# Kernel optimization log

Hardware: AMD Instinct MI355X
Metric: run time of the kernel (lower is better)

Reference implementation:

```python
import jax, jax.numpy as jnp
import numpy as np

ALPHA = 0.1
BETA = float(np.log(0.5 / 4 + 1.0))  # theta=0.5, layer=4


def setup_inputs() -> dict:
    key = jax.random.key(0)
    k = jax.random.split(key, 6)
    B, C, N, K = 1, 128, 40000, 16
    x = jax.random.normal(k[0], (B, C, N, 1), dtype=jnp.float32)
    x_0 = jax.random.normal(k[1], (B, N, C), dtype=jnp.float32)
    edge_index = jax.random.randint(k[2], (2, B, N, K), 0, N)
    W1 = jax.random.normal(k[3], (C, C), dtype=jnp.float32) * 0.05
    W2 = jax.random.normal(k[4], (C, C), dtype=jnp.float32) * 0.05
    bias = jax.random.uniform(k[5], (1, 1, C), dtype=jnp.float32)
    return {"x": x, "x_0": x_0, "edge_index": edge_index, "W1": W1, "W2": W2, "bias": bias}


def reference(x, x_0, edge_index, W1, W2, bias):
    # x: [B, C, N, 1]; x_0: [B, N, C]; edge_index: [2, B, N, K]
    B, C, N, _ = x.shape
    idx = edge_index[0]  # neighbor indices [B, N, K]
    self_idx = jnp.broadcast_to(jnp.arange(N, dtype=idx.dtype)[None, :, None], (B, N, 1))
    idx = jnp.concatenate([idx, self_idx], axis=-1)  # add self loops -> [B, N, K+1]
    deg = idx.shape[-1]  # constant degree K+1
    x2 = x[..., 0]  # [B, C, N]
    # irregular gather of neighbor features: [B, C, N, K+1]
    x_j = jax.vmap(lambda xb, ib: xb[:, ib])(x2, idx)
    aggr = x_j.sum(axis=-1) * (1.0 / deg)  # [B, C, N]
    aggr = jnp.swapaxes(aggr, 1, 2)  # [B, N, C]
    out = (aggr * ((1.0 - ALPHA) * (1.0 - BETA))
           + jnp.einsum('bnc,oc->bno', aggr, W1) * BETA
           + x_0 * (ALPHA * (1.0 - BETA))
           + jnp.einsum('bnc,oc->bno', x_0, W2) * BETA
           + bias)
    out = jax.nn.relu(out)
    return jnp.swapaxes(out, 1, 2)[..., None]  # [B, C, N, 1]
```

## Files before the change

kernel.cpp:

```cpp
#include <hip/hip_runtime.h>

#define N_NODES 40000
#define C_DIM   128
#define K_NBR   16

static constexpr float BETA_F  = 0.11778303565638346f;
static constexpr float C1_F    = 0.7939952679092549f;
static constexpr float C2_F    = 0.08822169643436166f;
static constexpr float INV_DEG = 1.0f / 17.0f;

typedef __attribute__((ext_vector_type(8))) short bf16x8;
typedef __attribute__((ext_vector_type(4))) float f32x4;

__device__ __forceinline__ unsigned pack_bf16x2(float a, float b) {
    unsigned ua = __float_as_uint(a), ub = __float_as_uint(b);
    ua += 0x7fffu + ((ua >> 16) & 1u);
    ub += 0x7fffu + ((ub >> 16) & 1u);
    return (ua >> 16) | (ub & 0xffff0000u);
}
__device__ __forceinline__ float bflo(unsigned u) { return __uint_as_float(u << 16); }
__device__ __forceinline__ float bfhi(unsigned u) { return __uint_as_float(u & 0xffff0000u); }

__global__ __launch_bounds__(256) void prep_kernel(
        const float* __restrict__ x,
        const float* __restrict__ W1,
        const float* __restrict__ W2,
        unsigned* __restrict__ xTb,
        unsigned short* __restrict__ WB) {
    __shared__ unsigned lds[32 * 65];

    const int b = blockIdx.x;
    const int tid = threadIdx.x;

    if (b < 128) {
        const int i = b * 256 + tid;
        const int frag = i >> 9, within = i & 511;
        const int lane = within >> 3, j = within & 7;
        const int otile = frag >> 3, kblk = frag & 7;
        const int o = otile * 16 + (lane & 15);
        const int c = kblk * 32 + ((lane >> 4) << 3) + j;
        float v;
        if (c < 128) {
            v = (BETA_F * W1[o * 128 + c] + (c == o ? C1_F : 0.0f)) * INV_DEG;
        } else {
            const int c2 = c - 128;
            v = BETA_F * W2[o * 128 + c2] + (c2 == o ? C2_F : 0.0f);
        }
        unsigned u = __float_as_uint(v);
        u += 0x7fffu + ((u >> 16) & 1u);
        WB[i] = (unsigned short)(u >> 16);
        return;
    }

    const int nb = (b - 128) * 32;

    const int c2 = tid >> 2;
    const int h  = tid & 3;
    const float* r0 = &x[(size_t)(2 * c2)     * N_NODES + nb + h * 8];
    const float* r1 = &x[(size_t)(2 * c2 + 1) * N_NODES + nb + h * 8];
    const float4 a0 = *(const float4*)(r0);
    const float4 a1 = *(const float4*)(r0 + 4);
    const float4 b0 = *(const float4*)(r1);
    const float4 b1 = *(const float4*)(r1 + 4);

    unsigned* lrow = &lds[h * 8 * 65 + c2];
    lrow[0 * 65] = pack_bf16x2(a0.x, b0.x);
    lrow[1 * 65] = pack_bf16x2(a0.y, b0.y);
    lrow[2 * 65] = pack_bf16x2(a0.z, b0.z);
    lrow[3 * 65] = pack_bf16x2(a0.w, b0.w);
    lrow[4 * 65] = pack_bf16x2(a1.x, b1.x);
    lrow[5 * 65] = pack_bf16x2(a1.y, b1.y);
    lrow[6 * 65] = pack_bf16x2(a1.z, b1.z);
    lrow[7 * 65] = pack_bf16x2(a1.w, b1.w);
    __syncthreads();

    const int n = tid >> 3, q = tid & 7;
    const unsigned* src = &lds[n * 65 + q * 8];
    unsigned* dst = &xTb[(size_t)(nb + n) * 64 + q * 8];
    *(uint4*)&dst[0] = make_uint4(src[0], src[1], src[2], src[3]);
    *(uint4*)&dst[4] = make_uint4(src[4], src[5], src[6], src[7]);
}

__global__ __launch_bounds__(256) void fused3_kernel(
        const unsigned* __restrict__ xTb,
        const float*    __restrict__ x0,
        const int*      __restrict__ e0,
        const bf16x8*   __restrict__ WB,
        const float*    __restrict__ bias,
        float*          __restrict__ out) {
    __shared__ unsigned y[32][132];
    __shared__ int eis[512];

    const int nb   = blockIdx.x * 32;
    const int tid  = threadIdx.x;
    const int lane = tid & 63;
    const int wid  = tid >> 6;

    eis[tid]       = e0[(size_t)nb * K_NBR + tid];
    eis[256 + tid] = e0[(size_t)nb * K_NBR + 256 + tid];
    __syncthreads();

    const int h  = lane >> 5;
    const int l5 = lane & 31;
#pragma unroll 2
    for (int p4 = 0; p4 < 4; ++p4) {
        const int local = wid * 8 + p4 * 2 + h;
        const int n = nb + local;
        const uint2 sv = *(const uint2*)&xTb[(size_t)n * 64 + 2 * l5];
        float a0 = bflo(sv.x), a1 = bfhi(sv.x);
        float a2 = bflo(sv.y), a3 = bfhi(sv.y);
        const int* ep = &eis[local * K_NBR];
#pragma unroll
        for (int k = 0; k < K_NBR; ++k) {
            const int j = ep[k];
            const uint2 v = *(const uint2*)&xTb[(size_t)j * 64 + 2 * l5];
            a0 += bflo(v.x); a1 += bfhi(v.x);
            a2 += bflo(v.y); a3 += bfhi(v.y);
        }
        *(uint2*)&y[local][2 * l5] =
            make_uint2(pack_bf16x2(a0, a1), pack_bf16x2(a2, a3));
        const float4 xv = *(const float4*)&x0[(size_t)n * C_DIM + 4 * l5];
        *(uint2*)&y[local][64 + 2 * l5] =
            make_uint2(pack_bf16x2(xv.x, xv.y), pack_bf16x2(xv.z, xv.w));
    }
    __syncthreads();

    const int nh = wid & 1;
    const int oh = wid >> 1;
    const int arow = nh * 16 + (lane & 15);
    const int acol = (lane >> 4) * 4;

    bf16x8 afrag[8];
#pragma unroll
    for (int kb = 0; kb < 8; ++kb)
        afrag[kb] = *(const bf16x8*)&y[arow][kb * 16 + acol];

    f32x4 acc[4];
#pragma unroll
    for (int t = 0; t < 4; ++t) {
        f32x4 a = {0.f, 0.f, 0.f, 0.f};
#pragma unroll
        for (int kb = 0; kb < 8; ++kb) {
            bf16x8 bv = WB[((oh * 4 + t) * 8 + kb) * 64 + lane];
            a = __builtin_amdgcn_mfma_f32_16x16x32_bf16(afrag[kb], bv, a, 0, 0, 0);
        }
        acc[t] = a;
    }

    const int rbase = nh * 16 + (lane >> 4) * 4;
#pragma unroll
    for (int t = 0; t < 4; ++t) {
        const int o = oh * 64 + t * 16 + (lane & 15);
        const float bo = bias[o];
        float4 res;
        res.x = fmaxf(acc[t][0] + bo, 0.0f);
        res.y = fmaxf(acc[t][1] + bo, 0.0f);
        res.z = fmaxf(acc[t][2] + bo, 0.0f);
        res.w = fmaxf(acc[t][3] + bo, 0.0f);
        *(float4*)&out[(size_t)o * N_NODES + nb + rbase] = res;
    }
}

extern "C" void kernel_launch(void* const* d_in, const int* in_sizes, int n_in,
                              void* d_out, int out_size, void* d_ws, size_t ws_size,
                              hipStream_t stream) {
    const float* x    = (const float*)d_in[0];
    const float* x0   = (const float*)d_in[1];
    const int*   ei   = (const int*)  d_in[2];
    const float* W1   = (const float*)d_in[3];
    const float* W2   = (const float*)d_in[4];
    const float* bias = (const float*)d_in[5];
    float* out = (float*)d_out;

    unsigned short* WB  = (unsigned short*)d_ws;
    unsigned*       xTb = (unsigned*)((char*)d_ws + 65536);

    hipLaunchKernelGGL(prep_kernel, dim3(1378), dim3(256), 0, stream,
                       x, W1, W2, xTb, WB);
    hipLaunchKernelGGL(fused3_kernel, dim3(1250), dim3(256), 0, stream,
                       xTb, x0, ei, (const bf16x8*)WB, bias, out);
}
```

Baseline: 40.86 us.

## Apply W1 before the gather so aggregation sums transformed features

Uses linearity to compute z1 = x·(βW1ᵀ/17 + c·I) per node first in the prep kernel, then gathers and sums z1 over neighbours. The second kernel only does the x0·W2 GEMM, with K halved, then adds the gathered sum. Weights are now converted to bf16 on the fly from fp32 in each block instead of in a separate prep pass, and the output is staged in LDS for coalesced transposed stores. This trades a larger first kernel, with an MFMA and per-block weight loads, for dropping the separate weight-packing step and halving the second GEMM. It also adds an extra LDS round trip and rounds the transformed features to bf16 before aggregation.

```diff
diff --git a/kernel.cpp b/kernel.cpp
--- a/kernel.cpp
+++ b/kernel.cpp
@@ -7,7 +7,10 @@
 static constexpr float BETA_F  = 0.11778303565638346f;
 static constexpr float C1_F    = 0.7939952679092549f;
 static constexpr float C2_F    = 0.08822169643436166f;
-static constexpr float INV_DEG = 1.0f / 17.0f;
+static constexpr float SCALE_X  = BETA_F / 17.0f;
+static constexpr float SCALE_X0 = BETA_F;
+static constexpr float CD1_F = C1_F / BETA_F;
+static constexpr float CD2_F = C2_F / BETA_F;
 
 typedef __attribute__((ext_vector_type(8))) short bf16x8;
 typedef __attribute__((ext_vector_type(4))) float f32x4;
@@ -21,143 +24,197 @@
 __device__ __forceinline__ float bflo(unsigned u) { return __uint_as_float(u << 16); }
 __device__ __forceinline__ float bfhi(unsigned u) { return __uint_as_float(u & 0xffff0000u); }
 
-__global__ __launch_bounds__(256) void prep_kernel(
+__device__ __forceinline__ bf16x8 pack_w8(const float* wp) {
+    const float4 wa = *(const float4*)wp;
+    const float4 wb = *(const float4*)(wp + 4);
+    unsigned u[4];
+    u[0] = pack_bf16x2(wa.x, wa.y);
+    u[1] = pack_bf16x2(wa.z, wa.w);
+    u[2] = pack_bf16x2(wb.x, wb.y);
+    u[3] = pack_bf16x2(wb.z, wb.w);
+    uint4 uu = make_uint4(u[0], u[1], u[2], u[3]);
+    return *(bf16x8*)&uu;
+}
+
+__global__ __launch_bounds__(256) void z1_kernel(
         const float* __restrict__ x,
         const float* __restrict__ W1,
-        const float* __restrict__ W2,
-        unsigned* __restrict__ xTb,
-        unsigned short* __restrict__ WB) {
-    __shared__ unsigned lds[32 * 65];
-
-    const int b = blockIdx.x;
+        unsigned* __restrict__ z1T) {
+    __shared__ unsigned xs[32 * 68];
+
+    const int nb  = blockIdx.x * 32;
     const int tid = threadIdx.x;
 
-    if (b < 128) {
-        const int i = b * 256 + tid;
-        const int frag = i >> 9, within = i & 511;
-        const int lane = within >> 3, j = within & 7;
-        const int otile = frag >> 3, kblk = frag & 7;
-        const int o = otile * 16 + (lane & 15);
-        const int c = kblk * 32 + ((lane >> 4) << 3) + j;
-        float v;
-        if (c < 128) {
-            v = (BETA_F * W1[o * 128 + c] + (c == o ? C1_F : 0.0f)) * INV_DEG;
-        } else {
-            const int c2 = c - 128;
-            v = BETA_F * W2[o * 128 + c2] + (c2 == o ? C2_F : 0.0f);
-        }
-        unsigned u = __float_as_uint(v);
-        u += 0x7fffu + ((u >> 16) & 1u);
-        WB[i] = (unsigned short)(u >> 16);
-        return;
-    }
-
-    const int nb = (b - 128) * 32;
-
-    const int c2 = tid >> 2;
-    const int h  = tid & 3;
-    const float* r0 = &x[(size_t)(2 * c2)     * N_NODES + nb + h * 8];
-    const float* r1 = &x[(size_t)(2 * c2 + 1) * N_NODES + nb + h * 8];
-    const float4 a0 = *(const float4*)(r0);
-    const float4 a1 = *(const float4*)(r0 + 4);
-    const float4 b0 = *(const float4*)(r1);
-    const float4 b1 = *(const float4*)(r1 + 4);
-
-    unsigned* lrow = &lds[h * 8 * 65 + c2];
-    lrow[0 * 65] = pack_bf16x2(a0.x, b0.x);
-    lrow[1 * 65] = pack_bf16x2(a0.y, b0.y);
-    lrow[2 * 65] = pack_bf16x2(a0.z, b0.z);
-    lrow[3 * 65] = pack_bf16x2(a0.w, b0.w);
-    lrow[4 * 65] = pack_bf16x2(a1.x, b1.x);
-    lrow[5 * 65] = pack_bf16x2(a1.y, b1.y);
-    lrow[6 * 65] = pack_bf16x2(a1.z, b1.z);
-    lrow[7 * 65] = pack_bf16x2(a1.w, b1.w);
-    __syncthreads();
-
-    const int n = tid >> 3, q = tid & 7;
-    const unsigned* src = &lds[n * 65 + q * 8];
-    unsigned* dst = &xTb[(size_t)(nb + n) * 64 + q * 8];
-    *(uint4*)&dst[0] = make_uint4(src[0], src[1], src[2], src[3]);
-    *(uint4*)&dst[4] = make_uint4(src[4], src[5], src[6], src[7]);
-}
-
-__global__ __launch_bounds__(256) void fused3_kernel(
-        const unsigned* __restrict__ xTb,
-        const float*    __restrict__ x0,
-        const int*      __restrict__ e0,
-        const bf16x8*   __restrict__ WB,
-        const float*    __restrict__ bias,
-        float*          __restrict__ out) {
-    __shared__ unsigned y[32][132];
-    __shared__ int eis[512];
-
-    const int nb   = blockIdx.x * 32;
-    const int tid  = threadIdx.x;
+    {
+        const int c2 = tid >> 2;
+        const int h  = tid & 3;
+        const float* r0 = &x[(size_t)(2 * c2)     * N_NODES + nb + h * 8];
+        const float* r1 = &x[(size_t)(2 * c2 + 1) * N_NODES + nb + h * 8];
+        const float4 a0 = *(const float4*)(r0);
+        const float4 a1 = *(const float4*)(r0 + 4);
+        const float4 b0 = *(const float4*)(r1);
+        const float4 b1 = *(const float4*)(r1 + 4);
+        unsigned* lr = &xs[(h * 8) * 68 + c2];
+        lr[0 * 68] = pack_bf16x2(a0.x * SCALE_X, b0.x * SCALE_X);
+        lr[1 * 68] = pack_bf16x2(a0.y * SCALE_X, b0.y * SCALE_X);
+        lr[2 * 68] = pack_bf16x2(a0.z * SCALE_X, b0.z * SCALE_X);
+        lr[3 * 68] = pack_bf16x2(a0.w * SCALE_X, b0.w * SCALE_X);
+        lr[4 * 68] = pack_bf16x2(a1.x * SCALE_X, b1.x * SCALE_X);
+        lr[5 * 68] = pack_bf16x2(a1.y * SCALE_X, b1.y * SCALE_X);
+        lr[6 * 68] = pack_bf16x2(a1.z * SCALE_X, b1.z * SCALE_X);
+        lr[7 * 68] = pack_bf16x2(a1.w * SCALE_X, b1.w * SCALE_X);
+    }
+    __syncthreads();
+
     const int lane = tid & 63;
     const int wid  = tid >> 6;
+    const int nh = wid & 1, oh = wid >> 1;
+    const int arow = nh * 16 + (lane & 15);
+    const int acol = (lane >> 4) * 4;
+
+    bf16x8 af[4];
+#pragma unroll
+    for (int kb = 0; kb < 4; ++kb)
+        af[kb] = *(const bf16x8*)&xs[arow * 68 + kb * 16 + acol];
+
+    const int ob = oh * 64 + (lane & 15);
+    const int cb = (lane >> 4) * 8;
+    const int rbase = nh * 16 + (lane >> 4) * 4;
+    const bool hi = (lane & 1) != 0;
+
+#pragma unroll
+    for (int t = 0; t < 4; ++t) {
+        const int o = ob + t * 16;
+        f32x4 a = {0.f, 0.f, 0.f, 0.f};
+#pragma unroll
+        for (int kb = 0; kb < 4; ++kb) {
+            const bf16x8 bw = pack_w8(&W1[(size_t)o * C_DIM + kb * 32 + cb]);
+            a = __builtin_amdgcn_mfma_f32_16x16x32_bf16(af[kb], bw, a, 0, 0, 0);
+        }
+#pragma unroll
+        for (int r = 0; r < 4; ++r) {
+            const int row = rbase + r;
+            const unsigned ux = xs[row * 68 + (o >> 1)];
+            float v = a[r] + CD1_F * (hi ? bfhi(ux) : bflo(ux));
+            const float vp = __shfl_xor(v, 1);
+            if (!hi) {
+                z1T[(size_t)(nb + row) * 64 + (o >> 1)] = pack_bf16x2(v, vp);
+            }
+        }
+    }
+}
+
+__global__ __launch_bounds__(256) void gather_kernel(
+        const unsigned* __restrict__ z1T,
+        const float*    __restrict__ x0,
+        const float*    __restrict__ W2,
+        const float*    __restrict__ bias,
+        const int*      __restrict__ e0,
+        float*          __restrict__ out) {
+    __shared__ int      eis[512];
+    __shared__ unsigned x0s[32 * 68];
+    __shared__ float    zbuf[32 * 132];
+
+    const int nb  = blockIdx.x * 32;
+    const int tid = threadIdx.x;
+    const int lane = tid & 63;
+    const int wid  = tid >> 6;
 
     eis[tid]       = e0[(size_t)nb * K_NBR + tid];
     eis[256 + tid] = e0[(size_t)nb * K_NBR + 256 + tid];
-    __syncthreads();
-
-    const int h  = lane >> 5;
-    const int l5 = lane & 31;
-#pragma unroll 2
-    for (int p4 = 0; p4 < 4; ++p4) {
-        const int local = wid * 8 + p4 * 2 + h;
+
+    {
+        const int n = tid >> 3, g = tid & 7;
+        const float* r = &x0[(size_t)(nb + n) * C_DIM + g * 16];
+        const float4 v0 = *(const float4*)(r);
+        const float4 v1 = *(const float4*)(r + 4);
+        const float4 v2 = *(const float4*)(r + 8);
+        const float4 v3 = *(const float4*)(r + 12);
+        uint4 ua, ub;
+        ua.x = pack_bf16x2(v0.x * SCALE_X0, v0.y * SCALE_X0);
+        ua.y = pack_bf16x2(v0.z * SCALE_X0, v0.w * SCALE_X0);
+        ua.z = pack_bf16x2(v1.x * SCALE_X0, v1.y * SCALE_X0);
+        ua.w = pack_bf16x2(v1.z * SCALE_X0, v1.w * SCALE_X0);
+        ub.x = pack_bf16x2(v2.x * SCALE_X0, v2.y * SCALE_X0);
+        ub.y = pack_bf16x2(v2.z * SCALE_X0, v2.w * SCALE_X0);
+        ub.z = pack_bf16x2(v3.x * SCALE_X0, v3.y * SCALE_X0);
+        ub.w = pack_bf16x2(v3.z * SCALE_X0, v3.w * SCALE_X0);
+        *(uint4*)&x0s[n * 68 + g * 8]     = ua;
+        *(uint4*)&x0s[n * 68 + g * 8 + 4] = ub;
+    }
+    __syncthreads();
+
+    const int nh = wid & 1, oh = wid >> 1;
+    const int arow = nh * 16 + (lane & 15);
+    const int acol = (lane >> 4) * 4;
+    bf16x8 af[4];
+#pragma unroll
+    for (int kb = 0; kb < 4; ++kb)
+        af[kb] = *(const bf16x8*)&x0s[arow * 68 + kb * 16 + acol];
+
+    const int ob = oh * 64 + (lane & 15);
+    const int cb = (lane >> 4) * 8;
+    f32x4 acc[4];
+#pragma unroll
+    for (int t = 0; t < 4; ++t) {
+        f32x4 a = {0.f, 0.f, 0.f, 0.f};
+#pragma unroll
+        for (int kb = 0; kb < 4; ++kb) {
+            const bf16x8 bw = pack_w8(&W2[(size_t)(ob + t * 16) * C_DIM + kb * 32 + cb]);
+            a = __builtin_amdgcn_mfma_f32_16x16x32_bf16(af[kb], bw, a, 0, 0, 0);
+        }
+        acc[t] = a;
+    }
+
+    const int hw = tid >> 5, l5 = tid & 31;
+#pragma unroll 1
+    for (int p = 0; p < 4; ++p) {
+        const int local = hw * 4 + p;
         const int n = nb + local;
-        const uint2 sv = *(const uint2*)&xTb[(size_t)n * 64 + 2 * l5];
-        float a0 = bflo(sv.x), a1 = bfhi(sv.x);
-        float a2 = bflo(sv.y), a3 = bfhi(sv.y);
+        const uint2 sv = *(const uint2*)&z1T[(size_t)n * 64 + 2 * l5];
+        float s0 = bflo(sv.x), s1 = bfhi(sv.x);
+        float s2 = bflo(sv.y), s3 = bfhi(sv.y);
         const int* ep = &eis[local * K_NBR];
 #pragma unroll
         for (int k = 0; k < K_NBR; ++k) {
             const int j = ep[k];
-            const uint2 v = *(const uint2*)&xTb[(size_t)j * 64 + 2 * l5];
-            a0 += bflo(v.x); a1 += bfhi(v.x);
-            a2 += bflo(v.y); a3 += bfhi(v.y);
-        }
-        *(uint2*)&y[local][2 * l5] =
-            make_uint2(pack_bf16x2(a0, a1), pack_bf16x2(a2, a3));
-        const float4 xv = *(const float4*)&x0[(size_t)n * C_DIM + 4 * l5];
-        *(uint2*)&y[local][64 + 2 * l5] =
-            make_uint2(pack_bf16x2(xv.x, xv.y), pack_bf16x2(xv.z, xv.w));
-    }
-    __syncthreads();
-
-    const int nh = wid & 1;
-    const int oh = wid >> 1;
-    const int arow = nh * 16 + (lane & 15);
-    const int acol = (lane >> 4) * 4;
-
-    bf16x8 afrag[8];
-#pragma unroll
-    for (int kb = 0; kb < 8; ++kb)
-        afrag[kb] = *(const bf16x8*)&y[arow][kb * 16 + acol];
-
-    f32x4 acc[4];
+            const uint2 v = *(const uint2*)&z1T[(size_t)j * 64 + 2 * l5];
+            s0 += bflo(v.x); s1 += bfhi(v.x);
+            s2 += bflo(v.y); s3 += bfhi(v.y);
+        }
+        *(f32x4*)&zbuf[local * 132 + 4 * l5] = (f32x4){s0, s1, s2, s3};
+    }
+    __syncthreads();
+
+    const int rbase = nh * 16 + (lane >> 4) * 4;
+    const bool hi = (lane & 1) != 0;
 #pragma unroll
     for (int t = 0; t < 4; ++t) {
-        f32x4 a = {0.f, 0.f, 0.f, 0.f};
-#pragma unroll
-        for (int kb = 0; kb < 8; ++kb) {
-            bf16x8 bv = WB[((oh * 4 + t) * 8 + kb) * 64 + lane];
-            a = __builtin_amdgcn_mfma_f32_16x16x32_bf16(afrag[kb], bv, a, 0, 0, 0);
-        }
-        acc[t] = a;
-    }
-
-    const int rbase = nh * 16 + (lane >> 4) * 4;
-#pragma unroll
-    for (int t = 0; t < 4; ++t) {
-        const int o = oh * 64 + t * 16 + (lane & 15);
+        const int o = ob + t * 16;
         const float bo = bias[o];
-        float4 res;
-        res.x = fmaxf(acc[t][0] + bo, 0.0f);
-        res.y = fmaxf(acc[t][1] + bo, 0.0f);
-        res.z = fmaxf(acc[t][2] + bo, 0.0f);
-        res.w = fmaxf(acc[t][3] + bo, 0.0f);
-        *(float4*)&out[(size_t)o * N_NODES + nb + rbase] = res;
+#pragma unroll
+        for (int r = 0; r < 4; ++r) {
+            const int row = rbase + r;
+            const unsigned ux = x0s[row * 68 + (o >> 1)];
+            const float x0v = hi ? bfhi(ux) : bflo(ux);
+            float v = zbuf[row * 132 + o] + acc[t][r] + CD2_F * x0v + bo;
+            zbuf[row * 132 + o] = v > 0.0f ? v : 0.0f;
+        }
+    }
+    __syncthreads();
+
+    const int o  = tid >> 1;
+    const int hh = tid & 1;
+    float* op = &out[(size_t)o * N_NODES + nb + hh * 16];
+#pragma unroll
+    for (int m = 0; m < 4; ++m) {
+        const int i = 4 * m;
+        float4 v;
+        v.x = zbuf[(hh * 16 + i + 0) * 132 + o];
+        v.y = zbuf[(hh * 16 + i + 1) * 132 + o];
+        v.z = zbuf[(hh * 16 + i + 2) * 132 + o];
+        v.w = zbuf[(hh * 16 + i + 3) * 132 + o];
+        *(float4*)(op + i) = v;
     }
 }
 
@@ -172,11 +229,10 @@
     const float* bias = (const float*)d_in[5];
     float* out = (float*)d_out;
 
-    unsigned short* WB  = (unsigned short*)d_ws;
-    unsigned*       xTb = (unsigned*)((char*)d_ws + 65536);
-
-    hipLaunchKernelGGL(prep_kernel, dim3(1378), dim3(256), 0, stream,
-                       x, W1, W2, xTb, WB);
-    hipLaunchKernelGGL(fused3_kernel, dim3(1250), dim3(256), 0, stream,
-                       xTb, x0, ei, (const bf16x8*)WB, bias, out);
-}
+    unsigned* z1T = (unsigned*)d_ws;
+
+    hipLaunchKernelGGL(z1_kernel, dim3(1250), dim3(256), 0, stream,
+                       x, W1, z1T);
+    hipLaunchKernelGGL(gather_kernel, dim3(1250), dim3(256), 0, stream,
+                       z1T, x0, W2, bias, ei, out);
+}
```

Measured after the change: 70.78 us. 73.2% more time.

## Remap gather threads to 8 lanes per node with register-held neighbor indices

Applied to the files above, without the earlier changes.

The neighbor-gather phase now gives each node 8 threads. Each thread covers 16-byte-spaced channel chunks over 4 passes, and the node's 16 neighbor indices are held in registers instead of re-read from LDS. The x0 conversion is split into its own upfront step, where each thread loads 64 contiguous bytes. The goal is to cut LDS index reads and change the memory access pattern of the gathers. In exchange, each gathered row is now read as 8-byte pieces spread across 8 lanes and 4 passes, rather than one wide coalesced read per half-wave, and register pressure rises.

```diff
diff --git a/kernel.cpp b/kernel.cpp
--- a/kernel.cpp
+++ b/kernel.cpp
@@ -81,7 +81,7 @@
     *(uint4*)&dst[4] = make_uint4(src[4], src[5], src[6], src[7]);
 }
 
-__global__ __launch_bounds__(256) void fused3_kernel(
+__global__ __launch_bounds__(256) void fused4_kernel(
         const unsigned* __restrict__ xTb,
         const float*    __restrict__ x0,
         const int*      __restrict__ e0,
@@ -100,28 +100,41 @@
     eis[256 + tid] = e0[(size_t)nb * K_NBR + 256 + tid];
     __syncthreads();
 
-    const int h  = lane >> 5;
-    const int l5 = lane & 31;
-#pragma unroll 2
-    for (int p4 = 0; p4 < 4; ++p4) {
-        const int local = wid * 8 + p4 * 2 + h;
-        const int n = nb + local;
-        const uint2 sv = *(const uint2*)&xTb[(size_t)n * 64 + 2 * l5];
-        float a0 = bflo(sv.x), a1 = bfhi(sv.x);
-        float a2 = bflo(sv.y), a3 = bfhi(sv.y);
-        const int* ep = &eis[local * K_NBR];
+    const int node = tid >> 3;
+    const int g8   = tid & 7;
+    {
+        const float* r = &x0[(size_t)(nb + node) * C_DIM + g8 * 16];
+        const float4 v0 = *(const float4*)(r);
+        const float4 v1 = *(const float4*)(r + 4);
+        const float4 v2 = *(const float4*)(r + 8);
+        const float4 v3 = *(const float4*)(r + 12);
+        uint4 ua, ub;
+        ua.x = pack_bf16x2(v0.x, v0.y);  ua.y = pack_bf16x2(v0.z, v0.w);
+        ua.z = pack_bf16x2(v1.x, v1.y);  ua.w = pack_bf16x2(v1.z, v1.w);
+        ub.x = pack_bf16x2(v2.x, v2.y);  ub.y = pack_bf16x2(v2.z, v2.w);
+        ub.z = pack_bf16x2(v3.x, v3.y);  ub.w = pack_bf16x2(v3.z, v3.w);
+        *(uint4*)&y[node][64 + g8 * 8]     = ua;
+        *(uint4*)&y[node][64 + g8 * 8 + 4] = ub;
+    }
+
+    int jreg[K_NBR];
+#pragma unroll
+    for (int k = 0; k < K_NBR; ++k) jreg[k] = eis[node * K_NBR + k];
+
+#pragma unroll 1
+    for (int q = 0; q < 4; ++q) {
+        const int off = q * 16 + 2 * g8;
+        const uint2 sv = *(const uint2*)&xTb[(size_t)(nb + node) * 64 + off];
+        float s0 = bflo(sv.x), s1 = bfhi(sv.x);
+        float s2 = bflo(sv.y), s3 = bfhi(sv.y);
 #pragma unroll
         for (int k = 0; k < K_NBR; ++k) {
-            const int j = ep[k];
-            const uint2 v = *(const uint2*)&xTb[(size_t)j * 64 + 2 * l5];
-            a0 += bflo(v.x); a1 += bfhi(v.x);
-            a2 += bflo(v.y); a3 += bfhi(v.y);
+            const uint2 v = *(const uint2*)&xTb[(size_t)jreg[k] * 64 + off];
+            s0 += bflo(v.x); s1 += bfhi(v.x);
+            s2 += bflo(v.y); s3 += bfhi(v.y);
         }
-        *(uint2*)&y[local][2 * l5] =
-            make_uint2(pack_bf16x2(a0, a1), pack_bf16x2(a2, a3));
-        const float4 xv = *(const float4*)&x0[(size_t)n * C_DIM + 4 * l5];
-        *(uint2*)&y[local][64 + 2 * l5] =
-            make_uint2(pack_bf16x2(xv.x, xv.y), pack_bf16x2(xv.z, xv.w));
+        *(uint2*)&y[node][off] =
+            make_uint2(pack_bf16x2(s0, s1), pack_bf16x2(s2, s3));
     }
     __syncthreads();
 
@@ -177,6 +190,6 @@
 
     hipLaunchKernelGGL(prep_kernel, dim3(1378), dim3(256), 0, stream,
                        x, W1, W2, xTb, WB);
-    hipLaunchKernelGGL(fused3_kernel, dim3(1250), dim3(256), 0, stream,
+    hipLaunchKernelGGL(fused4_kernel, dim3(1250), dim3(256), 0, stream,
                        xTb, x0, ei, (const bf16x8*)WB, bias, out);
 }
```

Result: no change. 40.63 us, median of 2 (-0.6%).
